# Performance work log

Hardware: AMD Instinct MI355X
Metric: run time of the kernel (lower is better)

## Reference

```python
import jax, jax.numpy as jnp
import numpy as np

B, SQ, SKV, D, H, DH, P = 8, 2048, 2048, 1024, 8, 128, 1024
LN_EPS = 1e-3  # keras LayerNormalization default


def _glorot(key, shape):
    fan_in, fan_out = shape[-2], shape[-1]
    lim = np.sqrt(6.0 / (fan_in + fan_out))
    return jax.random.uniform(key, shape, jnp.float32, -lim, lim)


def _layernorm(x, gamma, beta, eps=LN_EPS):
    mu = jnp.mean(x, axis=-1, keepdims=True)
    var = jnp.mean(jnp.square(x - mu), axis=-1, keepdims=True)
    return (x - mu) * jax.lax.rsqrt(var + eps) * gamma + beta


def setup_inputs() -> dict:
    key = jax.random.key(0)
    ks = jax.random.split(key, 8)
    return {
        "query": jax.random.normal(ks[0], (B, SQ, D), jnp.float32),
        "value": jax.random.normal(ks[1], (B, SKV, D), jnp.float32),
        "W1": _glorot(ks[2], (H, D, DH)),   # per-head query proj (stacked)
        "W2": _glorot(ks[3], (H, D, DH)),   # per-head key proj
        "W3": _glorot(ks[4], (H, D, DH)),   # per-head value proj
        "Wp": _glorot(ks[5], (H * DH, P)),  # output projection
        "bp": jnp.zeros((P,), jnp.float32),
        "Wt": _glorot(ks[6], (P, P)),       # transform (relu FFN)
        "bt": jnp.zeros((P,), jnp.float32),
        "g1": jnp.ones((P,), jnp.float32),
        "b1": jnp.zeros((P,), jnp.float32),
        "g2": jnp.ones((P,), jnp.float32),
        "b2": jnp.zeros((P,), jnp.float32),
    }


def reference(query, value, W1, W2, W3, Wp, bp, Wt, bt, g1, b1, g2, b2):
    # batched multi-head attention (original loops over heads; math identical)
    q = jnp.einsum("bsd,hde->bhse", query, W1)   # [B,H,SQ,DH]
    k = jnp.einsum("btd,hde->bhte", value, W2)   # [B,H,SKV,DH]
    v = jnp.einsum("btd,hde->bhte", value, W3)   # [B,H,SKV,DH]
    scale = 1.0 / jnp.sqrt(jnp.asarray(DH, jnp.float32))
    scores = jnp.einsum("bhse,bhte->bhst", q, k) * scale
    attn = jax.nn.softmax(scores, axis=-1)
    ctx = jnp.einsum("bhst,bhte->bhse", attn, v)  # [B,H,SQ,DH]
    # concat heads along feature axis
    cat = ctx.transpose(0, 2, 1, 3).reshape(B, SQ, H * DH)
    # project + residual + layernorm (dropout inactive: rate=0 / inference)
    proj = cat @ Wp + bp + query
    proj = _layernorm(proj, g1, b1)
    # relu transform + residual + layernorm
    t = jax.nn.relu(proj @ Wt + bt) + proj
    return _layernorm(t, g2, b2)
```

## Files before the change

kernel.cpp:

```cpp
#include <hip/hip_runtime.h>
#include <hip/hip_bf16.h>


typedef __bf16 bf16x8 __attribute__((ext_vector_type(8)));
typedef float  f32x4  __attribute__((ext_vector_type(4)));
typedef float  f32x16 __attribute__((ext_vector_type(16)));
typedef unsigned u32x4 __attribute__((ext_vector_type(4)));

#define GLDS16(g, l)                                                         \
  __builtin_amdgcn_global_load_lds(                                          \
      (__attribute__((address_space(1))) void*)(g),                          \
      (__attribute__((address_space(3))) void*)(l), 16, 0, 0)

__device__ __forceinline__ unsigned short f2bfu(float f) {
  unsigned int u = __builtin_bit_cast(unsigned int, f);
  u += 0x7fffu + ((u >> 16) & 1u);
  return (unsigned short)(u >> 16);
}
__device__ __forceinline__ float bfu2f(unsigned short u) {
  return __builtin_bit_cast(float, (unsigned int)u << 16);
}

__global__ __launch_bounds__(256) void cast_f32_bf16(
    const float* __restrict__ in, unsigned short* __restrict__ out, int n) {
  int i = (blockIdx.x * 256 + threadIdx.x) * 4;
  int stride = gridDim.x * 256 * 4;
  for (; i < n; i += stride) {
    float4 v = *(const float4*)(in + i);
    ushort4 o;
    o.x = f2bfu(v.x); o.y = f2bfu(v.y); o.z = f2bfu(v.z); o.w = f2bfu(v.w);
    *(ushort4*)(out + i) = o;
  }
}

__global__ __launch_bounds__(256) void transpose_cast(
    const float* __restrict__ in, unsigned short* __restrict__ out,
    int R, int C) {
  int b = blockIdx.z;
  in  += (size_t)b * R * C;
  out += (size_t)b * R * C;
  __shared__ float tile[32][33];
  int tx = threadIdx.x, ty = threadIdx.y;
  int c0 = blockIdx.x * 32, r0 = blockIdx.y * 32;
#pragma unroll
  for (int j = 0; j < 4; j++)
    tile[ty + j * 8][tx] = in[(size_t)(r0 + ty + j * 8) * C + c0 + tx];
  __syncthreads();
#pragma unroll
  for (int j = 0; j < 4; j++)
    out[(size_t)(c0 + ty + j * 8) * R + r0 + tx] = f2bfu(tile[tx][ty + j * 8]);
}

template <int MODE>
__global__ __launch_bounds__(512, 2) void gemm256(
    const unsigned short* __restrict__ A, const unsigned short* __restrict__ Bt,
    void* __restrict__ out, const float* __restrict__ bias,
    const void* __restrict__ extra, float scale,
    long strideA, long strideB, long strideO, int ntiles) {
  int bz = blockIdx.z;
  A  += (size_t)bz * strideA;
  Bt += (size_t)bz * strideB;
  int nb = gridDim.x;
  int qq = nb >> 3;
  int lin = blockIdx.x;
  int sw = (lin & 7) * qq + (lin >> 3);
  int nt = sw % ntiles, mt = sw / ntiles;
  int m0 = mt * 256, n0 = nt * 256;
  int tid = threadIdx.x;
  int wid = tid >> 6, lane = tid & 63;
  int l15 = lane & 15, l4 = lane >> 4;
  int wm = (wid >> 2) * 128, wn = (wid & 3) * 64;

  __shared__ alignas(16) char lds[131072];

  f32x4 acc[8][4];
#pragma unroll
  for (int i = 0; i < 8; i++)
#pragma unroll
    for (int j = 0; j < 4; j++) acc[i][j] = (f32x4){0.f, 0.f, 0.f, 0.f};

  const char* gA = (const char*)A + (size_t)m0 * 2048;
  const char* gB = (const char*)Bt + (size_t)n0 * 2048;

  auto STAGE = [&](int buf, int t) {
    char* ab = lds + buf * 65536;
    char* bb = ab + 32768;
#pragma unroll
    for (int i = 0; i < 4; i++) {
      int s = i * 512 + tid;
      int row = s >> 3;
      int g = (s & 7) ^ (row & 7);
      unsigned dst = (unsigned)((i * 512 + (tid & ~63)) * 16);
      GLDS16(gA + (size_t)row * 2048 + t * 128 + g * 16, ab + dst);
      GLDS16(gB + (size_t)row * 2048 + t * 128 + g * 16, bb + dst);
    }
  };

  STAGE(0, 0);
  for (int t = 0; t < 16; t++) {
    __builtin_amdgcn_sched_barrier(0);
    __builtin_amdgcn_s_barrier();
    if (t < 15) {
      STAGE((t + 1) & 1, t + 1);
      asm volatile("s_waitcnt vmcnt(8)" ::: "memory");
    } else {
      asm volatile("s_waitcnt vmcnt(0)" ::: "memory");
    }
    __builtin_amdgcn_s_barrier();
    __builtin_amdgcn_sched_barrier(0);

    const char* ab = lds + (t & 1) * 65536;
    const char* bb = ab + 32768;
#pragma unroll
    for (int kk = 0; kk < 2; kk++) {
      bf16x8 bfr[4];
#pragma unroll
      for (int nf = 0; nf < 4; nf++) {
        int r = wn + nf * 16 + l15;
        bfr[nf] = *(const bf16x8*)(bb + r * 128 + (((kk * 4 + l4) ^ (r & 7)) << 4));
      }
#pragma unroll
      for (int mh = 0; mh < 2; mh++) {
        bf16x8 af[4];
#pragma unroll
        for (int mf = 0; mf < 4; mf++) {
          int r = wm + mh * 64 + mf * 16 + l15;
          af[mf] = *(const bf16x8*)(ab + r * 128 + (((kk * 4 + l4) ^ (r & 7)) << 4));
        }
        __builtin_amdgcn_s_setprio(1);
#pragma unroll
        for (int mf = 0; mf < 4; mf++)
#pragma unroll
          for (int nf = 0; nf < 4; nf++)
            acc[mh * 4 + mf][nf] = __builtin_amdgcn_mfma_f32_16x16x32_bf16(
                af[mf], bfr[nf], acc[mh * 4 + mf][nf], 0, 0, 0);
        __builtin_amdgcn_s_setprio(0);
      }
    }
  }

#pragma unroll
  for (int mi = 0; mi < 8; mi++)
#pragma unroll
    for (int nf = 0; nf < 4; nf++)
#pragma unroll
      for (int r = 0; r < 4; r++) {
        int gm = m0 + wm + mi * 16 + l4 * 4 + r;
        int gn = n0 + wn + nf * 16 + l15;
        float v = acc[mi][nf][r];
        if constexpr (MODE == 0) {
          int b = gm >> 11, s = gm & 2047, h = gn >> 7, e = gn & 127;
          ((unsigned short*)out)[((((size_t)b * 8 + h) * 2048 + s) << 7) + e] =
              f2bfu(v * scale);
        } else if constexpr (MODE == 1) {
          ((unsigned short*)out + (size_t)bz * strideO)[(size_t)gm * 2048 + gn] =
              f2bfu(v);
        } else if constexpr (MODE == 2) {
          float r2 = v + bias[gn] + ((const float*)extra)[(size_t)gm * 1024 + gn];
          ((float*)out)[(size_t)gm * 1024 + gn] = r2;
        } else {
          float pl = bfu2f(((const unsigned short*)extra)[(size_t)gm * 1024 + gn]);
          float r2 = fmaxf(v + bias[gn], 0.0f) + pl;
          ((float*)out)[(size_t)gm * 1024 + gn] = r2;
        }
      }
}

__global__ __launch_bounds__(512) void fa_kernel(
    const unsigned short* __restrict__ Qh,
    const unsigned short* __restrict__ Kh,
    const unsigned short* __restrict__ Vt,
    unsigned short* __restrict__ catO) {
  int h = blockIdx.x, qt = blockIdx.y, b = blockIdx.z;
  int tid = threadIdx.x, wid = tid >> 6, lane = tid & 63;
  int q31 = lane & 31, hi = lane >> 5;

  __shared__ alignas(16) char lds[65536];

  const char* gK = (const char*)(Kh + (((size_t)b * 8 + h) * 2048) * 128);
  const char* gV = (const char*)(Vt + ((size_t)b * 1024 + h * 128) * 2048);

  bf16x8 qf[8];
  {
    const char* gQ = (const char*)(Qh + (((size_t)b * 8 + h) * 2048
                        + (size_t)qt * 256 + wid * 32 + q31) * 128);
#pragma unroll
    for (int ks = 0; ks < 8; ks++)
      qf[ks] = *(const bf16x8*)(gQ + ks * 32 + hi * 16);
  }

  f32x16 o[4];
#pragma unroll
  for (int et = 0; et < 4; et++)
#pragma unroll
    for (int r = 0; r < 16; r++) o[et][r] = 0.f;
  float lacc0 = 0.f, lacc1 = 0.f;

  auto STAGE_K = [&](int buf, int kt) {
    char* kb = lds + buf * 16384;
#pragma unroll
    for (int pass = 0; pass < 2; pass++) {
      int c = pass * 512 + tid;
      int row = c >> 4, ch = c & 15;
      int g = ch ^ (row & 15);
      GLDS16(gK + (size_t)(kt * 64 + row) * 256 + g * 16,
             kb + (pass * 512 + (tid & ~63)) * 16);
    }
  };
  auto STAGE_V = [&](int buf, int kt) {
    char* vb = lds + 32768 + buf * 16384;
#pragma unroll
    for (int pass = 0; pass < 2; pass++) {
      int c = pass * 512 + tid;
      int row = c >> 4, g = c & 15;
      int gp = g ^ (row & 15);
      int e = ((gp >> 3) << 6) + row;
      GLDS16(gV + (size_t)e * 4096 + kt * 128 + (gp & 7) * 16,
             vb + (pass * 512 + (tid & ~63)) * 16);
    }
  };
  auto QK = [&](int buf, f32x16& r0, f32x16& r1) {
    const char* kb = lds + buf * 16384;
#pragma unroll
    for (int r = 0; r < 16; r++) { r0[r] = 0.f; r1[r] = 0.f; }
    __builtin_amdgcn_s_setprio(1);
#pragma unroll
    for (int ks = 0; ks < 8; ks++) {
      int g = ((2 * ks + hi) ^ (q31 & 15)) << 4;
      bf16x8 k0 = *(const bf16x8*)(kb + q31 * 256 + g);
      bf16x8 k1 = *(const bf16x8*)(kb + (q31 + 32) * 256 + g);
      r0 = __builtin_amdgcn_mfma_f32_32x32x16_bf16(k0, qf[ks], r0, 0, 0, 0);
      r1 = __builtin_amdgcn_mfma_f32_32x32x16_bf16(k1, qf[ks], r1, 0, 0, 0);
    }
    __builtin_amdgcn_s_setprio(0);
  };
  auto SOFT_PV = [&](int buf, f32x16& s0, f32x16& s1) {
    float p[32];
#pragma unroll
    for (int r = 0; r < 16; r++) p[r] = __builtin_amdgcn_exp2f(s0[r]);
#pragma unroll
    for (int r = 0; r < 16; r++) p[16 + r] = __builtin_amdgcn_exp2f(s1[r]);
#pragma unroll
    for (int r = 0; r < 16; r++) { lacc0 += p[r]; lacc1 += p[16 + r]; }
    bf16x8 pa[4];
#pragma unroll
    for (int g = 0; g < 4; g++) {
      unsigned a0, a1, b0, b1;
      float p0 = p[g * 8 + 0], p1 = p[g * 8 + 1], p2 = p[g * 8 + 2], p3 = p[g * 8 + 3];
      float p4 = p[g * 8 + 4], p5 = p[g * 8 + 5], p6 = p[g * 8 + 6], p7 = p[g * 8 + 7];
      asm("v_cvt_pk_bf16_f32 %0, %1, %2" : "=v"(a0) : "v"(p0), "v"(p1));
      asm("v_cvt_pk_bf16_f32 %0, %1, %2" : "=v"(b0) : "v"(p4), "v"(p5));
      asm("v_cvt_pk_bf16_f32 %0, %1, %2" : "=v"(a1) : "v"(p2), "v"(p3));
      asm("v_cvt_pk_bf16_f32 %0, %1, %2" : "=v"(b1) : "v"(p6), "v"(p7));
      asm volatile("v_permlane32_swap_b32 %0, %1" : "+v"(a0), "+v"(b0));
      asm volatile("v_permlane32_swap_b32 %0, %1" : "+v"(a1), "+v"(b1));
      u32x4 w; w[0] = a0; w[1] = a1; w[2] = b0; w[3] = b1;
      pa[g] = __builtin_bit_cast(bf16x8, w);
    }
    const char* vb = lds + 32768 + buf * 16384;
    __builtin_amdgcn_s_setprio(1);
#pragma unroll
    for (int et = 0; et < 4; et++) {
      int row = (et & 1) * 32 + q31;
      int gb = (et >> 1) * 8;
#pragma unroll
      for (int ks = 0; ks < 4; ks++) {
        bf16x8 vf = *(const bf16x8*)(vb + row * 256 +
                        (((gb + 2 * ks + hi) ^ (row & 15)) << 4));
        o[et] = __builtin_amdgcn_mfma_f32_32x32x16_bf16(vf, pa[ks], o[et], 0, 0, 0);
      }
    }
    __builtin_amdgcn_s_setprio(0);
  };

  STAGE_K(0, 0); STAGE_K(1, 1); STAGE_V(0, 0);
  __syncthreads();
  f32x16 sA0, sA1, sB0, sB1;
  QK(0, sA0, sA1);

  for (int kt = 0; kt < 32; kt += 2) {
    __syncthreads();
    if (kt < 30) STAGE_K(kt & 1, kt + 2);
    if (kt < 31) STAGE_V((kt + 1) & 1, kt + 1);
    if (kt < 31) QK((kt + 1) & 1, sB0, sB1);
    SOFT_PV(kt & 1, sA0, sA1);
    __syncthreads();
    if (kt + 1 < 30) STAGE_K((kt + 1) & 1, kt + 3);
    if (kt + 1 < 31) STAGE_V(kt & 1, kt + 2);
    if (kt + 1 < 31) QK(kt & 1, sA0, sA1);
    SOFT_PV((kt + 1) & 1, sB0, sB1);
  }

  float lacc = lacc0 + lacc1;
  lacc += __shfl_xor(lacc, 32);
  float linv = 1.0f / lacc;
  __syncthreads();
  char* reg = lds + wid * 8192;
  int swz = (lane & 7) << 4;
#pragma unroll
  for (int et = 0; et < 4; et++)
#pragma unroll
    for (int pr = 0; pr < 8; pr++) {
      float lo = o[et][2 * pr] * linv, hf = o[et][2 * pr + 1] * linv;
      unsigned w;
      asm("v_cvt_pk_bf16_f32 %0, %1, %2" : "=v"(w) : "v"(lo), "v"(hf));
      int e = et * 32 + 8 * (pr >> 1) + 4 * hi + (pr & 1) * 2;
      *(unsigned*)(reg + q31 * 256 + ((e * 2) ^ swz)) = w;
    }
  size_t orow = (size_t)b * 2048 + (size_t)qt * 256 + wid * 32;
#pragma unroll
  for (int pass = 0; pass < 8; pass++) {
    int n = pass * 64 + lane;
    int q = n >> 4, ch = n & 15;
    bf16x8 v = *(const bf16x8*)(reg + q * 256 + ((ch * 16) ^ ((q & 7) << 4)));
    *(bf16x8*)((char*)(catO + (orow + q) * 1024 + h * 128) + ch * 16) = v;
  }
}

template <int OUT_BF16>
__global__ __launch_bounds__(256) void ln_kernel(
    const float* __restrict__ in, const float* __restrict__ g,
    const float* __restrict__ be, void* __restrict__ out) {
  int row = blockIdx.x;
  int tid = threadIdx.x;
  float4 v = ((const float4*)(in + (size_t)row * 1024))[tid];
  float s = v.x + v.y + v.z + v.w;
  float sq = v.x * v.x + v.y * v.y + v.z * v.z + v.w * v.w;
#pragma unroll
  for (int m = 1; m < 64; m <<= 1) {
    s += __shfl_xor(s, m);
    sq += __shfl_xor(sq, m);
  }
  __shared__ float ws[8];
  int wid = tid >> 6, lane = tid & 63;
  if (lane == 0) { ws[wid] = s; ws[wid + 4] = sq; }
  __syncthreads();
  s = ws[0] + ws[1] + ws[2] + ws[3];
  sq = ws[4] + ws[5] + ws[6] + ws[7];
  float mu = s * (1.0f / 1024.0f);
  float var = sq * (1.0f / 1024.0f) - mu * mu;
  float rs = rsqrtf(var + 1e-3f);
  float4 gg = ((const float4*)g)[tid];
  float4 bb = ((const float4*)be)[tid];
  float y0 = (v.x - mu) * rs * gg.x + bb.x;
  float y1 = (v.y - mu) * rs * gg.y + bb.y;
  float y2 = (v.z - mu) * rs * gg.z + bb.z;
  float y3 = (v.w - mu) * rs * gg.w + bb.w;
  if constexpr (OUT_BF16) {
    ushort4 ov;
    ov.x = f2bfu(y0); ov.y = f2bfu(y1); ov.z = f2bfu(y2); ov.w = f2bfu(y3);
    ((ushort4*)out)[(size_t)row * 256 + tid] = ov;
  } else {
    float4 ov = {y0, y1, y2, y3};
    ((float4*)out)[(size_t)row * 256 + tid] = ov;
  }
}

extern "C" void kernel_launch(void* const* d_in, const int* in_sizes, int n_in,
                              void* d_out, int out_size, void* d_ws, size_t ws_size,
                              hipStream_t stream) {
  const float* query = (const float*)d_in[0];
  const float* value = (const float*)d_in[1];
  const float* W1 = (const float*)d_in[2];
  const float* W2 = (const float*)d_in[3];
  const float* W3 = (const float*)d_in[4];
  const float* Wp = (const float*)d_in[5];
  const float* bp = (const float*)d_in[6];
  const float* Wt = (const float*)d_in[7];
  const float* bt = (const float*)d_in[8];
  const float* g1 = (const float*)d_in[9];
  const float* b1 = (const float*)d_in[10];
  const float* g2 = (const float*)d_in[11];
  const float* b2 = (const float*)d_in[12];

  char* ws = (char*)d_ws;
  unsigned short* qbf  = (unsigned short*)(ws + 0);
  unsigned short* vbf  = (unsigned short*)(ws + 33554432);
  unsigned short* Qh   = (unsigned short*)(ws + 67108864);
  unsigned short* Kh   = (unsigned short*)(ws + 100663296);
  unsigned short* Vt   = (unsigned short*)(ws + 134217728);
  unsigned short* Wq_t = (unsigned short*)(ws + 167772160);
  unsigned short* Wk_t = (unsigned short*)(ws + 169869312);
  unsigned short* Wv_t = (unsigned short*)(ws + 171966464);
  unsigned short* Wp_t = (unsigned short*)(ws + 174063616);
  unsigned short* Wt_t = (unsigned short*)(ws + 176160768);
  unsigned short* cat_ = qbf;
  float*          projf = (float*)(ws + 67108864);
  unsigned short* pln  = vbf;

  const int NE = 16384 * 1024;
  cast_f32_bf16<<<8192, 256, 0, stream>>>(query, qbf, NE);
  cast_f32_bf16<<<8192, 256, 0, stream>>>(value, vbf, NE);

  dim3 tb(32, 8);
  transpose_cast<<<dim3(4, 32, 8), tb, 0, stream>>>(W1, Wq_t, 1024, 128);
  transpose_cast<<<dim3(4, 32, 8), tb, 0, stream>>>(W2, Wk_t, 1024, 128);
  transpose_cast<<<dim3(4, 32, 8), tb, 0, stream>>>(W3, Wv_t, 1024, 128);
  transpose_cast<<<dim3(32, 32, 1), tb, 0, stream>>>(Wp, Wp_t, 1024, 1024);
  transpose_cast<<<dim3(32, 32, 1), tb, 0, stream>>>(Wt, Wt_t, 1024, 1024);

  const float QSCALE = 0.08838834764831845f * 1.4426950408889634f;
  gemm256<0><<<dim3(256, 1, 1), 512, 0, stream>>>(qbf, Wq_t, Qh, nullptr, nullptr,
                                                  QSCALE, 0, 0, 0, 4);
  gemm256<0><<<dim3(256, 1, 1), 512, 0, stream>>>(vbf, Wk_t, Kh, nullptr, nullptr,
                                                  1.0f, 0, 0, 0, 4);
  gemm256<1><<<dim3(32, 1, 8), 512, 0, stream>>>(Wv_t, vbf, Vt, nullptr, nullptr,
                                                 1.0f, 0, 2048L * 1024L, 1024L * 2048L, 8);
  fa_kernel<<<dim3(8, 8, 8), 512, 0, stream>>>(Qh, Kh, Vt, cat_);
  gemm256<2><<<dim3(256, 1, 1), 512, 0, stream>>>(cat_, Wp_t, projf, bp, query,
                                                  1.0f, 0, 0, 0, 4);
  ln_kernel<1><<<16384, 256, 0, stream>>>(projf, g1, b1, pln);
  gemm256<3><<<dim3(256, 1, 1), 512, 0, stream>>>(pln, Wt_t, projf, bt, pln,
                                                  1.0f, 0, 0, 0, 4);
  ln_kernel<0><<<16384, 256, 0, stream>>>(projf, g2, b2, (float*)d_out);
}
```

Measured before the change: 431.1 us.

## Batch prep launches, merge Q/K GEMMs, deepen FA pipeline, bf16 intermediates

The two input casts and the five weight transposes are each merged into fewer launches, and the Q and K projection GEMMs run as one launch using blockIdx.z. The flash-attention kernel moves to a 4-deep LDS ring with explicit vmcnt waits and drops setprio. The projection and FFN GEMM outputs are stored as bf16 instead of fp32 before each layernorm, which halves that traffic. The bf16 residual and pre-LN intermediates add rounding error, and the larger LDS use in attention may lower occupancy.

```diff
diff --git a/kernel.cpp b/kernel.cpp
--- a/kernel.cpp
+++ b/kernel.cpp
@@ -21,8 +21,11 @@
   return __builtin_bit_cast(float, (unsigned int)u << 16);
 }
 
-__global__ __launch_bounds__(256) void cast_f32_bf16(
-    const float* __restrict__ in, unsigned short* __restrict__ out, int n) {
+__global__ __launch_bounds__(256) void cast2_f32_bf16(
+    const float* __restrict__ in0, unsigned short* __restrict__ out0,
+    const float* __restrict__ in1, unsigned short* __restrict__ out1, int n) {
+  const float* in = blockIdx.z ? in1 : in0;
+  unsigned short* out = blockIdx.z ? out1 : out0;
   int i = (blockIdx.x * 256 + threadIdx.x) * 4;
   int stride = gridDim.x * 256 * 4;
   for (; i < n; i += stride) {
@@ -33,12 +36,8 @@
   }
 }
 
-__global__ __launch_bounds__(256) void transpose_cast(
-    const float* __restrict__ in, unsigned short* __restrict__ out,
-    int R, int C) {
-  int b = blockIdx.z;
-  in  += (size_t)b * R * C;
-  out += (size_t)b * R * C;
+__device__ __forceinline__ void tc_body(const float* in, unsigned short* out,
+                                        int R, int C) {
   __shared__ float tile[32][33];
   int tx = threadIdx.x, ty = threadIdx.y;
   int c0 = blockIdx.x * 32, r0 = blockIdx.y * 32;
@@ -49,17 +48,36 @@
 #pragma unroll
   for (int j = 0; j < 4; j++)
     out[(size_t)(c0 + ty + j * 8) * R + r0 + tx] = f2bfu(tile[tx][ty + j * 8]);
+}
+
+__global__ __launch_bounds__(256) void transpose_heads(
+    const float* __restrict__ W1, const float* __restrict__ W2,
+    const float* __restrict__ W3, unsigned short* __restrict__ O1,
+    unsigned short* __restrict__ O2, unsigned short* __restrict__ O3) {
+  int z = blockIdx.z, t = z >> 3, s = z & 7;
+  const float* in = (t == 0 ? W1 : t == 1 ? W2 : W3) + (size_t)s * 1024 * 128;
+  unsigned short* out = (t == 0 ? O1 : t == 1 ? O2 : O3) + (size_t)s * 1024 * 128;
+  tc_body(in, out, 1024, 128);
+}
+
+__global__ __launch_bounds__(256) void transpose_sq(
+    const float* __restrict__ Wp, const float* __restrict__ Wt,
+    unsigned short* __restrict__ Op, unsigned short* __restrict__ Ot) {
+  const float* in = blockIdx.z ? Wt : Wp;
+  unsigned short* out = blockIdx.z ? Ot : Op;
+  tc_body(in, out, 1024, 1024);
 }
 
 template <int MODE>
 __global__ __launch_bounds__(512, 2) void gemm256(
     const unsigned short* __restrict__ A, const unsigned short* __restrict__ Bt,
     void* __restrict__ out, const float* __restrict__ bias,
-    const void* __restrict__ extra, float scale,
+    const void* __restrict__ extra, float scale, float scale1,
     long strideA, long strideB, long strideO, int ntiles) {
   int bz = blockIdx.z;
   A  += (size_t)bz * strideA;
   Bt += (size_t)bz * strideB;
+  float sc = bz ? scale1 : scale;
   int nb = gridDim.x;
   int qq = nb >> 3;
   int lin = blockIdx.x;
@@ -139,6 +157,7 @@
     }
   }
 
+  unsigned short* outp = (unsigned short*)out + (size_t)bz * strideO;
 #pragma unroll
   for (int mi = 0; mi < 8; mi++)
 #pragma unroll
@@ -150,18 +169,15 @@
         float v = acc[mi][nf][r];
         if constexpr (MODE == 0) {
           int b = gm >> 11, s = gm & 2047, h = gn >> 7, e = gn & 127;
-          ((unsigned short*)out)[((((size_t)b * 8 + h) * 2048 + s) << 7) + e] =
-              f2bfu(v * scale);
+          outp[((((size_t)b * 8 + h) * 2048 + s) << 7) + e] = f2bfu(v * sc);
         } else if constexpr (MODE == 1) {
-          ((unsigned short*)out + (size_t)bz * strideO)[(size_t)gm * 2048 + gn] =
-              f2bfu(v);
+          outp[(size_t)gm * 2048 + gn] = f2bfu(v);
         } else if constexpr (MODE == 2) {
           float r2 = v + bias[gn] + ((const float*)extra)[(size_t)gm * 1024 + gn];
-          ((float*)out)[(size_t)gm * 1024 + gn] = r2;
+          outp[(size_t)gm * 1024 + gn] = f2bfu(r2);
         } else {
           float pl = bfu2f(((const unsigned short*)extra)[(size_t)gm * 1024 + gn]);
-          float r2 = fmaxf(v + bias[gn], 0.0f) + pl;
-          ((float*)out)[(size_t)gm * 1024 + gn] = r2;
+          outp[(size_t)gm * 1024 + gn] = f2bfu(fmaxf(v + bias[gn], 0.0f) + pl);
         }
       }
 }
@@ -175,7 +191,7 @@
   int tid = threadIdx.x, wid = tid >> 6, lane = tid & 63;
   int q31 = lane & 31, hi = lane >> 5;
 
-  __shared__ alignas(16) char lds[65536];
+  __shared__ alignas(16) char lds[131072];
 
   const char* gK = (const char*)(Kh + (((size_t)b * 8 + h) * 2048) * 128);
   const char* gV = (const char*)(Vt + ((size_t)b * 1024 + h * 128) * 2048);
@@ -196,8 +212,8 @@
     for (int r = 0; r < 16; r++) o[et][r] = 0.f;
   float lacc0 = 0.f, lacc1 = 0.f;
 
-  auto STAGE_K = [&](int buf, int kt) {
-    char* kb = lds + buf * 16384;
+  auto STAGE_K = [&](int kt) {
+    char* kb = lds + (kt & 3) * 16384;
 #pragma unroll
     for (int pass = 0; pass < 2; pass++) {
       int c = pass * 512 + tid;
@@ -207,8 +223,8 @@
              kb + (pass * 512 + (tid & ~63)) * 16);
     }
   };
-  auto STAGE_V = [&](int buf, int kt) {
-    char* vb = lds + 32768 + buf * 16384;
+  auto STAGE_V = [&](int kt) {
+    char* vb = lds + 65536 + (kt & 3) * 16384;
 #pragma unroll
     for (int pass = 0; pass < 2; pass++) {
       int c = pass * 512 + tid;
@@ -219,11 +235,10 @@
              vb + (pass * 512 + (tid & ~63)) * 16);
     }
   };
-  auto QK = [&](int buf, f32x16& r0, f32x16& r1) {
-    const char* kb = lds + buf * 16384;
+  auto QK = [&](int kt, f32x16& r0, f32x16& r1) {
+    const char* kb = lds + (kt & 3) * 16384;
 #pragma unroll
     for (int r = 0; r < 16; r++) { r0[r] = 0.f; r1[r] = 0.f; }
-    __builtin_amdgcn_s_setprio(1);
 #pragma unroll
     for (int ks = 0; ks < 8; ks++) {
       int g = ((2 * ks + hi) ^ (q31 & 15)) << 4;
@@ -232,9 +247,8 @@
       r0 = __builtin_amdgcn_mfma_f32_32x32x16_bf16(k0, qf[ks], r0, 0, 0, 0);
       r1 = __builtin_amdgcn_mfma_f32_32x32x16_bf16(k1, qf[ks], r1, 0, 0, 0);
     }
-    __builtin_amdgcn_s_setprio(0);
   };
-  auto SOFT_PV = [&](int buf, f32x16& s0, f32x16& s1) {
+  auto SOFT_PV = [&](int kt, f32x16& s0, f32x16& s1) {
     float p[32];
 #pragma unroll
     for (int r = 0; r < 16; r++) p[r] = __builtin_amdgcn_exp2f(s0[r]);
@@ -257,8 +271,7 @@
       u32x4 w; w[0] = a0; w[1] = a1; w[2] = b0; w[3] = b1;
       pa[g] = __builtin_bit_cast(bf16x8, w);
     }
-    const char* vb = lds + 32768 + buf * 16384;
-    __builtin_amdgcn_s_setprio(1);
+    const char* vb = lds + 65536 + (kt & 3) * 16384;
 #pragma unroll
     for (int et = 0; et < 4; et++) {
       int row = (et & 1) * 32 + q31;
@@ -270,25 +283,28 @@
         o[et] = __builtin_amdgcn_mfma_f32_32x32x16_bf16(vf, pa[ks], o[et], 0, 0, 0);
       }
     }
-    __builtin_amdgcn_s_setprio(0);
   };
 
-  STAGE_K(0, 0); STAGE_K(1, 1); STAGE_V(0, 0);
-  __syncthreads();
-  f32x16 sA0, sA1, sB0, sB1;
-  QK(0, sA0, sA1);
-
-  for (int kt = 0; kt < 32; kt += 2) {
-    __syncthreads();
-    if (kt < 30) STAGE_K(kt & 1, kt + 2);
-    if (kt < 31) STAGE_V((kt + 1) & 1, kt + 1);
-    if (kt < 31) QK((kt + 1) & 1, sB0, sB1);
-    SOFT_PV(kt & 1, sA0, sA1);
-    __syncthreads();
-    if (kt + 1 < 30) STAGE_K((kt + 1) & 1, kt + 3);
-    if (kt + 1 < 31) STAGE_V(kt & 1, kt + 2);
-    if (kt + 1 < 31) QK(kt & 1, sA0, sA1);
-    SOFT_PV((kt + 1) & 1, sB0, sB1);
+  STAGE_K(0); STAGE_V(0); STAGE_K(1); STAGE_V(1);
+
+  for (int w = 0; w < 16; w++) {
+    int kt = 2 * w;
+    asm volatile("s_waitcnt lgkmcnt(0)" ::: "memory");
+    __builtin_amdgcn_sched_barrier(0);
+    __builtin_amdgcn_s_barrier();
+    if (w < 15) {
+      STAGE_K(kt + 2); STAGE_V(kt + 2); STAGE_K(kt + 3); STAGE_V(kt + 3);
+      asm volatile("s_waitcnt vmcnt(8)" ::: "memory");
+    } else {
+      asm volatile("s_waitcnt vmcnt(0)" ::: "memory");
+    }
+    __builtin_amdgcn_s_barrier();
+    __builtin_amdgcn_sched_barrier(0);
+    f32x16 sA0, sA1, sB0, sB1;
+    QK(kt, sA0, sA1);
+    QK(kt + 1, sB0, sB1);
+    SOFT_PV(kt, sA0, sA1);
+    SOFT_PV(kt + 1, sB0, sB1);
   }
 
   float lacc = lacc0 + lacc1;
@@ -317,13 +333,19 @@
   }
 }
 
-template <int OUT_BF16>
+template <int IN_BF16, int OUT_BF16>
 __global__ __launch_bounds__(256) void ln_kernel(
-    const float* __restrict__ in, const float* __restrict__ g,
+    const void* __restrict__ in, const float* __restrict__ g,
     const float* __restrict__ be, void* __restrict__ out) {
   int row = blockIdx.x;
   int tid = threadIdx.x;
-  float4 v = ((const float4*)(in + (size_t)row * 1024))[tid];
+  float4 v;
+  if constexpr (IN_BF16) {
+    ushort4 u = ((const ushort4*)in)[(size_t)row * 256 + tid];
+    v.x = bfu2f(u.x); v.y = bfu2f(u.y); v.z = bfu2f(u.z); v.w = bfu2f(u.w);
+  } else {
+    v = ((const float4*)in)[(size_t)row * 256 + tid];
+  }
   float s = v.x + v.y + v.z + v.w;
   float sq = v.x * v.x + v.y * v.y + v.z * v.z + v.w * v.w;
 #pragma unroll
@@ -384,33 +406,30 @@
   unsigned short* Wv_t = (unsigned short*)(ws + 171966464);
   unsigned short* Wp_t = (unsigned short*)(ws + 174063616);
   unsigned short* Wt_t = (unsigned short*)(ws + 176160768);
-  unsigned short* cat_ = qbf;
-  float*          projf = (float*)(ws + 67108864);
-  unsigned short* pln  = vbf;
+  unsigned short* cat_  = qbf;
+  unsigned short* projb = Qh;
+  unsigned short* pln   = vbf;
+  unsigned short* tb    = Kh;
 
   const int NE = 16384 * 1024;
-  cast_f32_bf16<<<8192, 256, 0, stream>>>(query, qbf, NE);
-  cast_f32_bf16<<<8192, 256, 0, stream>>>(value, vbf, NE);
-
-  dim3 tb(32, 8);
-  transpose_cast<<<dim3(4, 32, 8), tb, 0, stream>>>(W1, Wq_t, 1024, 128);
-  transpose_cast<<<dim3(4, 32, 8), tb, 0, stream>>>(W2, Wk_t, 1024, 128);
-  transpose_cast<<<dim3(4, 32, 8), tb, 0, stream>>>(W3, Wv_t, 1024, 128);
-  transpose_cast<<<dim3(32, 32, 1), tb, 0, stream>>>(Wp, Wp_t, 1024, 1024);
-  transpose_cast<<<dim3(32, 32, 1), tb, 0, stream>>>(Wt, Wt_t, 1024, 1024);
+  cast2_f32_bf16<<<dim3(2048, 1, 2), 256, 0, stream>>>(query, qbf, value, vbf, NE);
+
+  dim3 tbk(32, 8);
+  transpose_heads<<<dim3(4, 32, 24), tbk, 0, stream>>>(W1, W2, W3, Wq_t, Wk_t, Wv_t);
+  transpose_sq<<<dim3(32, 32, 2), tbk, 0, stream>>>(Wp, Wt, Wp_t, Wt_t);
 
   const float QSCALE = 0.08838834764831845f * 1.4426950408889634f;
-  gemm256<0><<<dim3(256, 1, 1), 512, 0, stream>>>(qbf, Wq_t, Qh, nullptr, nullptr,
-                                                  QSCALE, 0, 0, 0, 4);
-  gemm256<0><<<dim3(256, 1, 1), 512, 0, stream>>>(vbf, Wk_t, Kh, nullptr, nullptr,
-                                                  1.0f, 0, 0, 0, 4);
-  gemm256<1><<<dim3(32, 1, 8), 512, 0, stream>>>(Wv_t, vbf, Vt, nullptr, nullptr,
-                                                 1.0f, 0, 2048L * 1024L, 1024L * 2048L, 8);
+  gemm256<0><<<dim3(256, 1, 2), 512, 0, stream>>>(
+      qbf, Wq_t, Qh, nullptr, nullptr, QSCALE, 1.0f,
+      16777216L, 1048576L, 16777216L, 4);
+  gemm256<1><<<dim3(32, 1, 8), 512, 0, stream>>>(
+      Wv_t, vbf, Vt, nullptr, nullptr, 1.0f, 1.0f,
+      0, 2048L * 1024L, 1024L * 2048L, 8);
   fa_kernel<<<dim3(8, 8, 8), 512, 0, stream>>>(Qh, Kh, Vt, cat_);
-  gemm256<2><<<dim3(256, 1, 1), 512, 0, stream>>>(cat_, Wp_t, projf, bp, query,
-                                                  1.0f, 0, 0, 0, 4);
-  ln_kernel<1><<<16384, 256, 0, stream>>>(projf, g1, b1, pln);
-  gemm256<3><<<dim3(256, 1, 1), 512, 0, stream>>>(pln, Wt_t, projf, bt, pln,
-                                                  1.0f, 0, 0, 0, 4);
-  ln_kernel<0><<<16384, 256, 0, stream>>>(projf, g2, b2, (float*)d_out);
-}
+  gemm256<2><<<dim3(256, 1, 1), 512, 0, stream>>>(
+      cat_, Wp_t, projb, bp, query, 1.0f, 1.0f, 0, 0, 0, 4);
+  ln_kernel<1, 1><<<16384, 256, 0, stream>>>(projb, g1, b1, pln);
+  gemm256<3><<<dim3(256, 1, 1), 512, 0, stream>>>(
+      pln, Wt_t, tb, bt, pln, 1.0f, 1.0f, 0, 0, 0, 4);
+  ln_kernel<1, 0><<<16384, 256, 0, stream>>>(tb, g2, b2, (float*)d_out);
+}
```

After: 409.8 us. -4.9%, faster.
